# Performance work log

Measured on AMD Instinct MI355X. Metric: run time of the kernel, lower is better.

## Reference

```python
import jax, jax.numpy as jnp
import numpy as np

B, S, F_IN = 128, 64, 32          # batch, window_size (seq), input features
E, L, H, HOR = 96, 4, 8, 24       # embed_dim, num_layers, num_heads, horizon
E2 = 2 * E                        # attention hidden size (conv output channels)
D = E2 // H                       # head_dim
FLAT = S * E2                     # flattened fc feature size


def _ln(x, scale, offset, eps=1e-5):
    mu = jnp.mean(x, axis=-1, keepdims=True)
    var = jnp.var(x, axis=-1, keepdims=True)
    return (x - mu) * jax.lax.rsqrt(var + eps) * scale + offset


def _gattention(h, qk_w, qk_b, mass_w, mass_b, v_w, v_b):
    b, s, _ = h.shape
    qk = (h @ qk_w + qk_b).reshape(b, s, H, D).transpose(0, 2, 1, 3)  # (b,h,s,d)
    # d^2 = |qi|^2 + |qj|^2 - 2 qi.qj  (GEMM identity; exact value is >= 0)
    sq = jnp.sum(qk * qk, axis=-1)                                    # (b,h,s)
    dot = jnp.einsum('bhid,bhjd->bhij', qk, qk)
    d2 = jnp.maximum(sq[:, :, :, None] + sq[:, :, None, :] - 2.0 * dot, 0.0) + 1e-6
    mass = jax.nn.softplus(h @ mass_w + mass_b).transpose(0, 2, 1)    # (b,h,s)
    scores = (mass[:, :, :, None] * mass[:, :, None, :]) / d2
    w = jax.nn.softmax(scores, axis=-1)
    v = (h @ v_w + v_b).reshape(b, s, H, D).transpose(0, 2, 1, 3)
    out = jnp.einsum('bhij,bhjd->bhid', w, v)
    return out.transpose(0, 2, 1, 3).reshape(b, s, E2)


def setup_inputs() -> dict:
    key = jax.random.key(0)
    ks = iter(jax.random.split(key, 16))
    r = lambda *shape: jax.random.normal(next(ks), shape, jnp.float32) * 0.02
    return dict(
        x=jax.random.normal(next(ks), (B, S, F_IN), jnp.float32),
        proj_w=r(F_IN, E), proj_b=jnp.zeros((E,), jnp.float32),
        ln0_s=jnp.ones((E,), jnp.float32), ln0_o=jnp.zeros((E,), jnp.float32),
        conv_w=r(4, 4, E, E2), conv_b=jnp.zeros((E2,), jnp.float32),
        ln1_s=jnp.ones((E2,), jnp.float32), ln1_o=jnp.zeros((E2,), jnp.float32),
        qk_w=r(L, E2, E2), qk_b=jnp.zeros((L, E2), jnp.float32),
        mass_w=r(L, E2, H), mass_b=jnp.zeros((L, H), jnp.float32),
        v_w=r(L, E2, E2), v_b=jnp.zeros((L, E2), jnp.float32),
        norm_s=jnp.ones((L, E2), jnp.float32), norm_o=jnp.zeros((L, E2), jnp.float32),
        mlp_w1=r(E2, 4 * E), mlp_b1=jnp.zeros((4 * E,), jnp.float32),
        mlp_w2=r(4 * E, E2), mlp_b2=jnp.zeros((E2,), jnp.float32),
        fc_w=r(FLAT, FLAT), fc_b=jnp.zeros((FLAT,), jnp.float32),
        ln2_s=jnp.ones((FLAT,), jnp.float32), ln2_o=jnp.zeros((FLAT,), jnp.float32),
        out_w=r(FLAT, HOR), out_b=jnp.zeros((HOR,), jnp.float32),
    )


def reference(x, proj_w, proj_b, ln0_s, ln0_o, conv_w, conv_b, ln1_s, ln1_o,
              qk_w, qk_b, mass_w, mass_b, v_w, v_b, norm_s, norm_o,
              mlp_w1, mlp_b1, mlp_w2, mlp_b2, fc_w, fc_b, ln2_s, ln2_o,
              out_w, out_b):
    # proj: Linear -> LN -> gelu
    h = jax.nn.gelu(_ln(x @ proj_w + proj_b, ln0_s, ln0_o))            # (B,S,E)
    # hk.Conv2D on rank-3 input: treated as a single unbatched HWC image
    y = jax.lax.conv_general_dilated(
        h[None], conv_w, window_strides=(1, 1), padding='SAME',
        dimension_numbers=('NHWC', 'HWIO', 'NHWC'))[0] + conv_b        # (B,S,E2)
    h = jax.nn.gelu(_ln(y, ln1_s, ln1_o))
    for i in range(L):
        a = _gattention(h, qk_w[i], qk_b[i], mass_w[i], mass_b[i], v_w[i], v_b[i])
        h = jax.nn.gelu(_ln(h + a, norm_s[i], norm_o[i]))
    h = h + (jax.nn.gelu(h @ mlp_w1 + mlp_b1) @ mlp_w2 + mlp_b2)
    f = _ln(jax.nn.gelu(h.reshape(B, FLAT) @ fc_w + fc_b), ln2_s, ln2_o)
    return f @ out_w + out_b                                           # (B,HOR)
```

## Files before the change

kernel.cpp:

```cpp
#include <hip/hip_runtime.h>
#include <math.h>

typedef __attribute__((ext_vector_type(8))) short short8;
typedef __attribute__((ext_vector_type(4))) float f32x4;

__device__ __forceinline__ unsigned short bf16_rne(float f) {
  union { float f; unsigned u; } x; x.f = f;
  unsigned r = x.u + 0x7FFFu + ((x.u >> 16) & 1u);
  return (unsigned short)(r >> 16);
}

__device__ __forceinline__ float gelu_f(float x) {
  float z = 0.7978845608028654f * (x + 0.044715f * x * x * x);
  z = fminf(fmaxf(z, -15.f), 15.f);
  float e = __expf(2.f * z);
  float th = (e - 1.f) / (e + 1.f);
  return 0.5f * x * (1.f + th);
}

__device__ __forceinline__ float softplus_f(float x) {
  return (x > 15.f) ? x : log1pf(__expf(x));
}

__device__ __forceinline__ float wave_sum(float v) {
  #pragma unroll
  for (int off = 32; off > 0; off >>= 1) v += __shfl_down(v, off, 64);
  return v;
}

__global__ __launch_bounds__(256) void proj_kern(
    const float* __restrict__ x, const float* __restrict__ w,
    const float* __restrict__ b, const float* __restrict__ s,
    const float* __restrict__ o, unsigned short* __restrict__ h0bf)
{
  int t = threadIdx.x, wave = t >> 6, l = t & 63;
  size_t row = (size_t)blockIdx.x * 4 + wave;
  const float* xr = x + row * 32;
  bool has2 = (l < 32);
  int c1 = l, c2 = has2 ? 64 + l : 0;
  float v1 = b[c1], v2 = b[c2];
  #pragma unroll
  for (int k = 0; k < 32; ++k) {
    float xv = xr[k];
    v1 += xv * w[k * 96 + c1];
    v2 += xv * w[k * 96 + c2];
  }
  if (!has2) v2 = 0.f;
  float sum = wave_sum(v1 + v2);
  float ssq = wave_sum(v1 * v1 + v2 * v2);
  sum = __shfl(sum, 0, 64); ssq = __shfl(ssq, 0, 64);
  float mu = sum / 96.f, var = ssq / 96.f - mu * mu;
  float inv = rsqrtf(var + 1e-5f);
  float f1 = gelu_f((v1 - mu) * inv * s[c1] + o[c1]);
  h0bf[row * 96 + c1] = bf16_rne(f1);
  if (has2) {
    float f2 = gelu_f((v2 - mu) * inv * s[c2] + o[c2]);
    h0bf[row * 96 + c2] = bf16_rne(f2);
  }
}

__global__ __launch_bounds__(256) void cvtw_kern(
    const float* __restrict__ cw, unsigned short* __restrict__ cwT)
{
  int e = blockIdx.x * 256 + threadIdx.x;
  int co = e % 192, rest = e / 192;
  int ci = rest % 96, tap = rest / 96;
  cwT[((size_t)tap * 192 + co) * 96 + ci] = bf16_rne(cw[e]);
}

__global__ __launch_bounds__(256) void conv_kern(
    const unsigned short* __restrict__ h0bf, const unsigned short* __restrict__ cwT,
    const float* __restrict__ cb, float* __restrict__ y)
{
  __shared__ unsigned short As[12 * 64 * 8];
  __shared__ unsigned short Ws[12 * 64 * 8];
  int t = threadIdx.x;
  int i = blockIdx.x;
  int n0 = blockIdx.y * 64;
  int wave = t >> 6, lane = t & 63, quad = lane >> 4, l16 = lane & 15;
  f32x4 zero4 = {0.f, 0.f, 0.f, 0.f};
  f32x4 acc[4];
  #pragma unroll
  for (int nt = 0; nt < 4; ++nt) acc[nt] = zero4;
  for (int tap = 0; tap < 16; ++tap) {
    int kh = tap >> 2, kw = tap & 3;
    int si = i + kh - 1;
    if (si < 0 || si >= 128) continue;
    {
      int j = t & 63, g = t >> 6;
      int sj = j + kw - 1;
      bool ok = (sj >= 0 && sj < 64);
      #pragma unroll
      for (int q = 0; q < 3; ++q) {
        int kb = g + 4 * q;
        short8 v = {0,0,0,0,0,0,0,0};
        if (ok) v = *(const short8*)(h0bf + (size_t)(si * 64 + sj) * 96 + kb * 8);
        *(short8*)(As + (kb * 64 + j) * 8) = v;
      }
    }
    {
      int n = t & 63, g = t >> 6;
      #pragma unroll
      for (int q = 0; q < 3; ++q) {
        int kb = g + 4 * q;
        *(short8*)(Ws + (kb * 64 + n) * 8) =
            *(const short8*)(cwT + ((size_t)tap * 192 + n0 + n) * 96 + kb * 8);
      }
    }
    __syncthreads();
    #pragma unroll
    for (int ks = 0; ks < 3; ++ks) {
      int kbq = ks * 4 + quad;
      short8 a = *(const short8*)(As + (kbq * 64 + wave * 16 + l16) * 8);
      #pragma unroll
      for (int nt = 0; nt < 4; ++nt) {
        short8 b = *(const short8*)(Ws + (kbq * 64 + nt * 16 + l16) * 8);
        acc[nt] = __builtin_amdgcn_mfma_f32_16x16x32_bf16(a, b, acc[nt], 0, 0, 0);
      }
    }
    __syncthreads();
  }
  #pragma unroll
  for (int nt = 0; nt < 4; ++nt) {
    int col = n0 + nt * 16 + l16;
    float bv = cb[col];
    #pragma unroll
    for (int r = 0; r < 4; ++r) {
      int row = wave * 16 + quad * 4 + r;
      y[(size_t)(i * 64 + row) * 192 + col] = acc[nt][r] + bv;
    }
  }
}

__global__ __launch_bounds__(256) void ln_act_kern(
    const float* __restrict__ y, const float* __restrict__ res,
    const float* __restrict__ s, const float* __restrict__ o,
    float* __restrict__ h32, unsigned short* __restrict__ hbf)
{
  int t = threadIdx.x, wave = t >> 6, l = t & 63;
  size_t base = ((size_t)blockIdx.x * 4 + wave) * 192;
  float v0 = y[base + l], v1 = y[base + 64 + l], v2 = y[base + 128 + l];
  if (res) { v0 += res[base + l]; v1 += res[base + 64 + l]; v2 += res[base + 128 + l]; }
  float sum = wave_sum(v0 + v1 + v2);
  float ssq = wave_sum(v0 * v0 + v1 * v1 + v2 * v2);
  sum = __shfl(sum, 0, 64); ssq = __shfl(ssq, 0, 64);
  float mu = sum * (1.f / 192.f);
  float var = ssq * (1.f / 192.f) - mu * mu;
  float inv = rsqrtf(var + 1e-5f);
  float f0 = gelu_f((v0 - mu) * inv * s[l] + o[l]);
  float f1 = gelu_f((v1 - mu) * inv * s[64 + l] + o[64 + l]);
  float f2 = gelu_f((v2 - mu) * inv * s[128 + l] + o[128 + l]);
  h32[base + l] = f0; h32[base + 64 + l] = f1; h32[base + 128 + l] = f2;
  hbf[base + l] = bf16_rne(f0); hbf[base + 64 + l] = bf16_rne(f1); hbf[base + 128 + l] = bf16_rne(f2);
}

__global__ __launch_bounds__(256) void gemm_qkv(
    const unsigned short* __restrict__ A,
    const float* __restrict__ qw, const float* __restrict__ qb,
    const float* __restrict__ vw, const float* __restrict__ vb,
    float* __restrict__ t_qk, float* __restrict__ t_v)
{
  __shared__ unsigned short As[8 * 64 * 8];
  __shared__ unsigned short Ws[8 * 64 * 8];
  int t = threadIdx.x;
  int m0 = blockIdx.x * 64;
  int ny = blockIdx.y;
  const float* W; const float* bias; float* outF; int n0;
  if (ny < 3) { W = qw; bias = qb; outF = t_qk; n0 = ny * 64; }
  else        { W = vw; bias = vb; outF = t_v;  n0 = (ny - 3) * 64; }
  int wave = t >> 6, lane = t & 63, quad = lane >> 4, l16 = lane & 15;
  f32x4 zero4 = {0.f, 0.f, 0.f, 0.f};
  f32x4 acc[4];
  #pragma unroll
  for (int nt = 0; nt < 4; ++nt) acc[nt] = zero4;
  for (int k0 = 0; k0 < 192; k0 += 64) {
    {
      int kb = t & 7, m = t >> 3;
      #pragma unroll
      for (int r = 0; r < 2; ++r) {
        int mm = m + r * 32;
        *(short8*)(As + (kb * 64 + mm) * 8) =
            *(const short8*)(A + (size_t)(m0 + mm) * 192 + k0 + kb * 8);
      }
    }
    {
      int n = t & 63, g = t >> 6;
      #pragma unroll
      for (int q = 0; q < 2; ++q) {
        int kb = g + 4 * q;
        short8 v;
        #pragma unroll
        for (int jj = 0; jj < 8; ++jj)
          v[jj] = (short)bf16_rne(W[(size_t)(k0 + kb * 8 + jj) * 192 + n0 + n]);
        *(short8*)(Ws + (kb * 64 + n) * 8) = v;
      }
    }
    __syncthreads();
    #pragma unroll
    for (int ks = 0; ks < 2; ++ks) {
      short8 a = *(const short8*)(As + ((ks * 4 + quad) * 64 + wave * 16 + l16) * 8);
      #pragma unroll
      for (int nt = 0; nt < 4; ++nt) {
        short8 b = *(const short8*)(Ws + ((ks * 4 + quad) * 64 + nt * 16 + l16) * 8);
        acc[nt] = __builtin_amdgcn_mfma_f32_16x16x32_bf16(a, b, acc[nt], 0, 0, 0);
      }
    }
    __syncthreads();
  }
  #pragma unroll
  for (int nt = 0; nt < 4; ++nt) {
    int col = n0 + nt * 16 + l16;
    float bv = bias[col];
    #pragma unroll
    for (int r = 0; r < 4; ++r) {
      int row = m0 + wave * 16 + quad * 4 + r;
      outF[(size_t)row * 192 + col] = acc[nt][r] + bv;
    }
  }
}

__global__ __launch_bounds__(256) void gemm_small(
    const unsigned short* __restrict__ A, int lda,
    const float* __restrict__ W, int ldw,
    const float* __restrict__ bias, const float* __restrict__ res,
    float* __restrict__ outF, unsigned short* __restrict__ outB,
    int K, int ldo, int act)
{
  __shared__ unsigned short As[8 * 64 * 8];
  __shared__ unsigned short Ws[8 * 64 * 8];
  int t = threadIdx.x;
  int m0 = blockIdx.x * 64, n0 = blockIdx.y * 64;
  int wave = t >> 6, lane = t & 63, quad = lane >> 4, l16 = lane & 15;
  f32x4 zero4 = {0.f, 0.f, 0.f, 0.f};
  f32x4 acc[4];
  #pragma unroll
  for (int nt = 0; nt < 4; ++nt) acc[nt] = zero4;
  for (int k0 = 0; k0 < K; k0 += 64) {
    {
      int kb = t & 7, m = t >> 3;
      #pragma unroll
      for (int r = 0; r < 2; ++r) {
        int mm = m + r * 32;
        *(short8*)(As + (kb * 64 + mm) * 8) =
            *(const short8*)(A + (size_t)(m0 + mm) * lda + k0 + kb * 8);
      }
    }
    {
      int n = t & 63, g = t >> 6;
      #pragma unroll
      for (int q = 0; q < 2; ++q) {
        int kb = g + 4 * q;
        short8 v;
        #pragma unroll
        for (int jj = 0; jj < 8; ++jj)
          v[jj] = (short)bf16_rne(W[(size_t)(k0 + kb * 8 + jj) * ldw + n0 + n]);
        *(short8*)(Ws + (kb * 64 + n) * 8) = v;
      }
    }
    __syncthreads();
    #pragma unroll
    for (int ks = 0; ks < 2; ++ks) {
      short8 a = *(const short8*)(As + ((ks * 4 + quad) * 64 + wave * 16 + l16) * 8);
      #pragma unroll
      for (int nt = 0; nt < 4; ++nt) {
        short8 b = *(const short8*)(Ws + ((ks * 4 + quad) * 64 + nt * 16 + l16) * 8);
        acc[nt] = __builtin_amdgcn_mfma_f32_16x16x32_bf16(a, b, acc[nt], 0, 0, 0);
      }
    }
    __syncthreads();
  }
  #pragma unroll
  for (int nt = 0; nt < 4; ++nt) {
    int col = n0 + nt * 16 + l16;
    float bv = bias[col];
    #pragma unroll
    for (int r = 0; r < 4; ++r) {
      int row = m0 + wave * 16 + quad * 4 + r;
      float v = acc[nt][r] + bv;
      if (act) v = gelu_f(v);
      if (res) v += res[(size_t)row * ldo + col];
      if (outF) outF[(size_t)row * ldo + col] = v;
      if (outB) outB[(size_t)row * ldo + col] = bf16_rne(v);
    }
  }
}

__global__ __launch_bounds__(256) void attn_core(
    const float* __restrict__ qk, const float* __restrict__ v,
    const float* __restrict__ h32, const float* __restrict__ mw,
    const float* __restrict__ mb, float* __restrict__ att)
{
  __shared__ float qs[64][25], vs[64][25];
  __shared__ float sqv[64], mm[64], inv64[64];
  __shared__ float sc[64][65];
  int t = threadIdx.x;
  int b = blockIdx.x >> 3, hh = blockIdx.x & 7;
  size_t base = ((size_t)b * 64) * 192 + hh * 24;
  for (int e = t; e < 1536; e += 256) {
    int r = e / 24, d = e - r * 24;
    qs[r][d] = qk[base + (size_t)r * 192 + d];
    vs[r][d] = v[base + (size_t)r * 192 + d];
  }
  {
    int r = t >> 2, q = t & 3;
    const float* hr = h32 + ((size_t)b * 64 + r) * 192 + q * 48;
    float dot = 0.f;
    #pragma unroll
    for (int kk = 0; kk < 48; ++kk) dot += hr[kk] * mw[(q * 48 + kk) * 8 + hh];
    dot += __shfl_down(dot, 2, 4);
    dot += __shfl_down(dot, 1, 4);
    if (q == 0) mm[r] = softplus_f(dot + mb[hh]);
  }
  __syncthreads();
  if (t < 64) {
    float s = 0.f;
    #pragma unroll
    for (int d = 0; d < 24; ++d) s += qs[t][d] * qs[t][d];
    sqv[t] = s;
  }
  __syncthreads();
  {
    int i = t & 63, g = t >> 6;
    float qi[24];
    #pragma unroll
    for (int d = 0; d < 24; ++d) qi[d] = qs[i][d];
    float sqi = sqv[i], mi = mm[i];
    for (int jj = 0; jj < 16; ++jj) {
      int j = g + jj * 4;
      float dot = 0.f;
      #pragma unroll
      for (int d = 0; d < 24; ++d) dot += qi[d] * qs[j][d];
      float d2 = fmaxf(sqi + sqv[j] - 2.f * dot, 0.f) + 1e-6f;
      sc[i][j] = mi * mm[j] / d2;
    }
  }
  __syncthreads();
  if (t < 64) {
    float mx = -1e30f;
    for (int j = 0; j < 64; ++j) mx = fmaxf(mx, sc[t][j]);
    float sum = 0.f;
    for (int j = 0; j < 64; ++j) { float e = __expf(sc[t][j] - mx); sc[t][j] = e; sum += e; }
    inv64[t] = 1.f / sum;
  }
  __syncthreads();
  {
    int i = t & 63, g = t >> 6;
    float a6[6] = {0,0,0,0,0,0};
    for (int j = 0; j < 64; ++j) {
      float w = sc[i][j];
      #pragma unroll
      for (int dd = 0; dd < 6; ++dd) a6[dd] += w * vs[j][g * 6 + dd];
    }
    float inv = inv64[i];
    #pragma unroll
    for (int dd = 0; dd < 6; ++dd)
      att[base + (size_t)i * 192 + g * 6 + dd] = a6[dd] * inv;
  }
}

__global__ __launch_bounds__(256) void gemm_fc(
    const unsigned short* __restrict__ A, const float* __restrict__ W,
    float* __restrict__ part)
{
  __shared__ unsigned short As[8 * 128 * 8];
  __shared__ unsigned short Bs[8 * 64 * 8];
  int t = threadIdx.x;
  int n0 = blockIdx.x * 64;
  int split = blockIdx.y;
  int wave = t >> 6, lane = t & 63, quad = lane >> 4, l16 = lane & 15;
  int wm = wave * 32;
  int a_kb = t & 7, a_m = t >> 3;
  int w_n4 = t & 15, w_kr = t >> 4;
  f32x4 zero4 = {0.f, 0.f, 0.f, 0.f};
  f32x4 acc[2][4];
  #pragma unroll
  for (int mt = 0; mt < 2; ++mt)
    #pragma unroll
    for (int nt = 0; nt < 4; ++nt) acc[mt][nt] = zero4;
  int k0 = split * 3072;
  for (int it = 0; it < 48; ++it, k0 += 64) {
    #pragma unroll
    for (int r = 0; r < 4; ++r) {
      int mm2 = a_m + r * 32;
      *(short8*)(As + (a_kb * 128 + mm2) * 8) =
          *(const short8*)(A + (size_t)mm2 * 12288 + k0 + a_kb * 8);
    }
    #pragma unroll
    for (int r = 0; r < 4; ++r) {
      int k = w_kr + 16 * r;
      f32x4 wv = *(const f32x4*)(W + (size_t)(k0 + k) * 12288 + n0 + w_n4 * 4);
      int kb = k >> 3, kj = k & 7;
      #pragma unroll
      for (int j = 0; j < 4; ++j)
        Bs[(kb * 64 + w_n4 * 4 + j) * 8 + kj] = bf16_rne(wv[j]);
    }
    __syncthreads();
    #pragma unroll
    for (int ks = 0; ks < 2; ++ks) {
      int kq = ks * 4 + quad;
      short8 a[2], b[4];
      #pragma unroll
      for (int mt = 0; mt < 2; ++mt)
        a[mt] = *(const short8*)(As + (kq * 128 + wm + mt * 16 + l16) * 8);
      #pragma unroll
      for (int nt = 0; nt < 4; ++nt)
        b[nt] = *(const short8*)(Bs + (kq * 64 + nt * 16 + l16) * 8);
      #pragma unroll
      for (int mt = 0; mt < 2; ++mt)
        #pragma unroll
        for (int nt = 0; nt < 4; ++nt)
          acc[mt][nt] = __builtin_amdgcn_mfma_f32_16x16x32_bf16(a[mt], b[nt], acc[mt][nt], 0, 0, 0);
    }
    __syncthreads();
  }
  float* po = part + (size_t)split * 128 * 12288;
  #pragma unroll
  for (int mt = 0; mt < 2; ++mt) {
    #pragma unroll
    for (int nt = 0; nt < 4; ++nt) {
      int col = n0 + nt * 16 + l16;
      #pragma unroll
      for (int r = 0; r < 4; ++r) {
        int row = wm + mt * 16 + quad * 4 + r;
        po[(size_t)row * 12288 + col] = acc[mt][nt][r];
      }
    }
  }
}

__global__ __launch_bounds__(256) void reduce_fc(
    const float* __restrict__ part, const float* __restrict__ fb,
    float* __restrict__ g)
{
  int i4 = blockIdx.x * 256 + threadIdx.x;
  const int S4 = 128 * 12288 / 4;
  const f32x4* p = (const f32x4*)part;
  f32x4 v = p[i4] + p[i4 + S4] + p[i4 + 2 * S4] + p[i4 + 3 * S4];
  int n = (i4 * 4) % 12288;
  f32x4 bb = *(const f32x4*)(fb + n);
  f32x4 o;
  #pragma unroll
  for (int c = 0; c < 4; ++c) o[c] = gelu_f(v[c] + bb[c]);
  ((f32x4*)g)[i4] = o;
}

__global__ __launch_bounds__(256) void final_kern(
    const float* __restrict__ g, const float* __restrict__ s,
    const float* __restrict__ o, const float* __restrict__ ow,
    const float* __restrict__ ob, float* __restrict__ out)
{
  int m = blockIdx.x, t = threadIdx.x;
  const float* gr = g + (size_t)m * 12288;
  float s1 = 0.f, s2 = 0.f;
  for (int k4 = t; k4 < 3072; k4 += 256) {
    f32x4 v = ((const f32x4*)gr)[k4];
    s1 += v[0] + v[1] + v[2] + v[3];
    s2 += v[0]*v[0] + v[1]*v[1] + v[2]*v[2] + v[3]*v[3];
  }
  s1 = wave_sum(s1); s2 = wave_sum(s2);
  __shared__ float a1[4], a2[4];
  int wv = t >> 6, ln = t & 63;
  if (ln == 0) { a1[wv] = s1; a2[wv] = s2; }
  __syncthreads();
  float sum = a1[0] + a1[1] + a1[2] + a1[3];
  float ssq = a2[0] + a2[1] + a2[2] + a2[3];
  float mu = sum / 12288.f, var = ssq / 12288.f - mu * mu;
  float inv = rsqrtf(var + 1e-5f);
  f32x4 acc6[6];
  #pragma unroll
  for (int j = 0; j < 6; ++j) acc6[j] = (f32x4){0.f,0.f,0.f,0.f};
  for (int k = t; k < 12288; k += 256) {
    float f = (gr[k] - mu) * inv * s[k] + o[k];
    const f32x4* owr = (const f32x4*)(ow + (size_t)k * 24);
    #pragma unroll
    for (int j = 0; j < 6; ++j) acc6[j] += f * owr[j];
  }
  __shared__ float red[4][24];
  #pragma unroll
  for (int j = 0; j < 6; ++j)
    #pragma unroll
    for (int c = 0; c < 4; ++c) {
      float v = wave_sum(acc6[j][c]);
      if (ln == 0) red[wv][j * 4 + c] = v;
    }
  __syncthreads();
  if (t < 24) out[m * 24 + t] = red[0][t] + red[1][t] + red[2][t] + red[3][t] + ob[t];
}

extern "C" void kernel_launch(void* const* d_in, const int* in_sizes, int n_in,
                              void* d_out, int out_size, void* d_ws, size_t ws_size,
                              hipStream_t stream) {
  const float* x      = (const float*)d_in[0];
  const float* proj_w = (const float*)d_in[1];
  const float* proj_b = (const float*)d_in[2];
  const float* ln0_s  = (const float*)d_in[3];
  const float* ln0_o  = (const float*)d_in[4];
  const float* conv_w = (const float*)d_in[5];
  const float* conv_b = (const float*)d_in[6];
  const float* ln1_s  = (const float*)d_in[7];
  const float* ln1_o  = (const float*)d_in[8];
  const float* qk_w   = (const float*)d_in[9];
  const float* qk_b   = (const float*)d_in[10];
  const float* mass_w = (const float*)d_in[11];
  const float* mass_b = (const float*)d_in[12];
  const float* v_w    = (const float*)d_in[13];
  const float* v_b    = (const float*)d_in[14];
  const float* norm_s = (const float*)d_in[15];
  const float* norm_o = (const float*)d_in[16];
  const float* mlp_w1 = (const float*)d_in[17];
  const float* mlp_b1 = (const float*)d_in[18];
  const float* mlp_w2 = (const float*)d_in[19];
  const float* mlp_b2 = (const float*)d_in[20];
  const float* fc_w   = (const float*)d_in[21];
  const float* fc_b   = (const float*)d_in[22];
  const float* ln2_s  = (const float*)d_in[23];
  const float* ln2_o  = (const float*)d_in[24];
  const float* out_w  = (const float*)d_in[25];
  const float* out_b  = (const float*)d_in[26];
  float* out = (float*)d_out;

  char* ws = (char*)d_ws;
  unsigned short* h0bf = (unsigned short*)(ws + 0);
  float* h32           = (float*)(ws + 1572864);
  unsigned short* hbf  = (unsigned short*)(ws + 7864320);
  unsigned short* cwT  = (unsigned short*)(ws + 11010048);
  char* sc = ws + 11599872;
  float* t_qk  = (float*)(sc);
  float* t_v   = (float*)(sc + 6291456);
  float* t_att = (float*)(sc + 12582912);
  unsigned short* hid_bf = (unsigned short*)(sc + 18874368);
  float* partials = (float*)sc;
  float* gbuf = h32;

  proj_kern<<<2048, 256, 0, stream>>>(x, proj_w, proj_b, ln0_s, ln0_o, h0bf);
  cvtw_kern<<<1152, 256, 0, stream>>>(conv_w, cwT);
  conv_kern<<<dim3(128, 3), 256, 0, stream>>>(h0bf, cwT, conv_b, t_att);
  ln_act_kern<<<2048, 256, 0, stream>>>(t_att, nullptr, ln1_s, ln1_o, h32, hbf);
  for (int l = 0; l < 4; ++l) {
    gemm_qkv<<<dim3(128, 6), 256, 0, stream>>>(hbf, qk_w + l * 36864, qk_b + l * 192,
        v_w + l * 36864, v_b + l * 192, t_qk, t_v);
    attn_core<<<1024, 256, 0, stream>>>(t_qk, t_v, h32, mass_w + l * 1536,
                                        mass_b + l * 8, t_att);
    ln_act_kern<<<2048, 256, 0, stream>>>(t_att, h32, norm_s + l * 192,
                                          norm_o + l * 192, h32, hbf);
  }
  gemm_small<<<dim3(128, 6), 256, 0, stream>>>(hbf, 192, mlp_w1, 384, mlp_b1,
      nullptr, (float*)nullptr, hid_bf, 192, 384, 1);
  gemm_small<<<dim3(128, 3), 256, 0, stream>>>(hid_bf, 384, mlp_w2, 192, mlp_b2,
      h32, h32, hbf, 384, 192, 0);
  gemm_fc<<<dim3(192, 4), 256, 0, stream>>>(hbf, fc_w, partials);
  reduce_fc<<<1536, 256, 0, stream>>>(partials, fc_b, gbuf);
  final_kern<<<128, 256, 0, stream>>>(gbuf, ln2_s, ln2_o, out_w, out_b, out);
}
```

Baseline: 1.150 ms.

## Fuse QKV projection and attention per layer, merge pre and final kernels

New measurement: 1.101 ms. 1.04x faster.

```diff
diff --git a/kernel.cpp b/kernel.cpp
--- a/kernel.cpp
+++ b/kernel.cpp
@@ -28,11 +28,19 @@
   return v;
 }
 
-__global__ __launch_bounds__(256) void proj_kern(
+__global__ __launch_bounds__(256) void pre_kern(
     const float* __restrict__ x, const float* __restrict__ w,
     const float* __restrict__ b, const float* __restrict__ s,
-    const float* __restrict__ o, unsigned short* __restrict__ h0bf)
-{
+    const float* __restrict__ o, unsigned short* __restrict__ h0bf,
+    const float* __restrict__ cw, unsigned short* __restrict__ cwT)
+{
+  if (blockIdx.x >= 2048) {
+    int e = (blockIdx.x - 2048) * 256 + threadIdx.x;
+    int co = e % 192, rest = e / 192;
+    int ci = rest % 96, tap = rest / 96;
+    cwT[((size_t)tap * 192 + co) * 96 + ci] = bf16_rne(cw[e]);
+    return;
+  }
   int t = threadIdx.x, wave = t >> 6, l = t & 63;
   size_t row = (size_t)blockIdx.x * 4 + wave;
   const float* xr = x + row * 32;
@@ -57,15 +65,6 @@
     float f2 = gelu_f((v2 - mu) * inv * s[c2] + o[c2]);
     h0bf[row * 96 + c2] = bf16_rne(f2);
   }
-}
-
-__global__ __launch_bounds__(256) void cvtw_kern(
-    const float* __restrict__ cw, unsigned short* __restrict__ cwT)
-{
-  int e = blockIdx.x * 256 + threadIdx.x;
-  int co = e % 192, rest = e / 192;
-  int ci = rest % 96, tap = rest / 96;
-  cwT[((size_t)tap * 192 + co) * 96 + ci] = bf16_rne(cw[e]);
 }
 
 __global__ __launch_bounds__(256) void conv_kern(
@@ -154,69 +153,225 @@
   hbf[base + l] = bf16_rne(f0); hbf[base + 64 + l] = bf16_rne(f1); hbf[base + 128 + l] = bf16_rne(f2);
 }
 
-__global__ __launch_bounds__(256) void gemm_qkv(
-    const unsigned short* __restrict__ A,
+__device__ __forceinline__ void stage_w(
+    unsigned short* Wt, const float* qw, const float* vw, const float* mw,
+    int half, int k0, int t)
+{
+  for (int c = t; c < 1664; c += 256) {
+    int kb = c / 208, n = c - kb * 208;
+    short8 v8;
+    if (n < 192) {
+      const float* src = (n < 96) ? (qw + half * 96 + n) : (vw + half * 96 + n - 96);
+      #pragma unroll
+      for (int jj = 0; jj < 8; ++jj)
+        v8[jj] = (short)bf16_rne(src[(size_t)(k0 + kb * 8 + jj) * 192]);
+    } else if (n < 196) {
+      const float* src = mw + half * 4 + (n - 192);
+      #pragma unroll
+      for (int jj = 0; jj < 8; ++jj)
+        v8[jj] = (short)bf16_rne(src[(size_t)(k0 + kb * 8 + jj) * 8]);
+    } else {
+      v8 = (short8){0,0,0,0,0,0,0,0};
+    }
+    *(short8*)(Wt + c * 8) = v8;
+  }
+}
+
+__global__ __launch_bounds__(256) void layer_attn(
+    const unsigned short* __restrict__ hbf,
     const float* __restrict__ qw, const float* __restrict__ qb,
     const float* __restrict__ vw, const float* __restrict__ vb,
-    float* __restrict__ t_qk, float* __restrict__ t_v)
-{
-  __shared__ unsigned short As[8 * 64 * 8];
-  __shared__ unsigned short Ws[8 * 64 * 8];
+    const float* __restrict__ mw, const float* __restrict__ mb,
+    float* __restrict__ att)
+{
+  extern __shared__ char smem[];
+  unsigned short* qk_lds = (unsigned short*)smem;
+  unsigned short* v_ldsp = (unsigned short*)(smem + 16384);
+  unsigned short* w_bfp  = (unsigned short*)(smem + 32768);
+  float* mmp = (float*)(smem + 65536);
+  float* sqp = (float*)(smem + 66560);
+  unsigned short* A_bf = (unsigned short*)smem;
+  unsigned short* Wt   = (unsigned short*)(smem + 24576);
+
   int t = threadIdx.x;
-  int m0 = blockIdx.x * 64;
-  int ny = blockIdx.y;
-  const float* W; const float* bias; float* outF; int n0;
-  if (ny < 3) { W = qw; bias = qb; outF = t_qk; n0 = ny * 64; }
-  else        { W = vw; bias = vb; outF = t_v;  n0 = (ny - 3) * 64; }
-  int wave = t >> 6, lane = t & 63, quad = lane >> 4, l16 = lane & 15;
-  f32x4 zero4 = {0.f, 0.f, 0.f, 0.f};
-  f32x4 acc[4];
-  #pragma unroll
-  for (int nt = 0; nt < 4; ++nt) acc[nt] = zero4;
-  for (int k0 = 0; k0 < 192; k0 += 64) {
-    {
-      int kb = t & 7, m = t >> 3;
-      #pragma unroll
-      for (int r = 0; r < 2; ++r) {
-        int mm = m + r * 32;
-        *(short8*)(As + (kb * 64 + mm) * 8) =
-            *(const short8*)(A + (size_t)(m0 + mm) * 192 + k0 + kb * 8);
-      }
-    }
-    {
-      int n = t & 63, g = t >> 6;
-      #pragma unroll
-      for (int q = 0; q < 2; ++q) {
-        int kb = g + 4 * q;
-        short8 v;
+  int bb = blockIdx.x >> 1, half = blockIdx.x & 1;
+  int wv = t >> 6, lane = t & 63, quad = lane >> 4, l16 = lane & 15;
+
+  for (int c = t; c < 1536; c += 256) {
+    int kb = c >> 6, m = c & 63;
+    *(short8*)(A_bf + c * 8) =
+        *(const short8*)(hbf + ((size_t)bb * 64 + m) * 192 + kb * 8);
+  }
+  stage_w(Wt, qw, vw, mw, half, 0, t);
+  __syncthreads();
+  f32x4 acc[13];
+  #pragma unroll
+  for (int i = 0; i < 13; ++i) acc[i] = (f32x4){0.f,0.f,0.f,0.f};
+  for (int kt = 0; kt < 3; ++kt) {
+    #pragma unroll
+    for (int ks = 0; ks < 2; ++ks) {
+      int kq = ks * 4 + quad;
+      short8 a = *(const short8*)(A_bf + ((kt * 8 + kq) * 64 + wv * 16 + l16) * 8);
+      #pragma unroll
+      for (int nt = 0; nt < 13; ++nt) {
+        short8 b = *(const short8*)(Wt + (kq * 208 + nt * 16 + l16) * 8);
+        acc[nt] = __builtin_amdgcn_mfma_f32_16x16x32_bf16(a, b, acc[nt], 0, 0, 0);
+      }
+    }
+    if (kt < 2) {
+      __syncthreads();
+      stage_w(Wt, qw, vw, mw, half, (kt + 1) * 64, t);
+      __syncthreads();
+    }
+  }
+  __syncthreads();
+
+  {
+    int zh = t >> 6, zs = t & 63;
+    *(short8*)(qk_lds + ((zh * 4 + 3) * 64 + zs) * 8) = (short8){0,0,0,0,0,0,0,0};
+  }
+  int row = wv * 16 + quad * 4;
+  #pragma unroll
+  for (int nt = 0; nt < 6; ++nt) {
+    int n = nt * 16 + l16;
+    int hl = n / 24, d = n - hl * 24;
+    float bqv = qb[half * 96 + n];
+    #pragma unroll
+    for (int r = 0; r < 4; ++r)
+      qk_lds[((hl * 4 + (d >> 3)) * 64 + row + r) * 8 + (d & 7)] =
+          bf16_rne(acc[nt][r] + bqv);
+  }
+  #pragma unroll
+  for (int nt = 0; nt < 6; ++nt) {
+    int n = nt * 16 + l16;
+    int hl = n / 24, d = n - hl * 24;
+    float bvv = vb[half * 96 + n];
+    #pragma unroll
+    for (int r = 0; r < 4; ++r) {
+      int sidx = row + r;
+      v_ldsp[((hl * 8 + (sidx >> 3)) * 32 + d) * 8 + (sidx & 7)] =
+          bf16_rne(acc[nt + 6][r] + bvv);
+    }
+  }
+  if (l16 < 4) {
+    float mbv = mb[half * 4 + l16];
+    #pragma unroll
+    for (int r = 0; r < 4; ++r)
+      mmp[(row + r) * 4 + l16] = softplus_f(acc[12][r] + mbv);
+  }
+  __syncthreads();
+
+  const unsigned short* qh = qk_lds + (wv * 4) * 64 * 8;
+  short8 frag[4];
+  #pragma unroll
+  for (int x2 = 0; x2 < 4; ++x2)
+    frag[x2] = *(const short8*)(qh + (quad * 64 + x2 * 16 + l16) * 8);
+  f32x4 s16[4][4];
+  #pragma unroll
+  for (int mt = 0; mt < 4; ++mt)
+    #pragma unroll
+    for (int nt = 0; nt < 4; ++nt)
+      s16[mt][nt] = __builtin_amdgcn_mfma_f32_16x16x32_bf16(
+          frag[mt], frag[nt], (f32x4){0.f,0.f,0.f,0.f}, 0, 0, 0);
+  float* sqh = sqp + wv * 64;
+  #pragma unroll
+  for (int mt = 0; mt < 4; ++mt)
+    #pragma unroll
+    for (int r = 0; r < 4; ++r)
+      if (l16 == quad * 4 + r) sqh[mt * 16 + l16] = s16[mt][mt][r];
+  __syncthreads();
+  f32x4 sqr[4], mr[4];
+  float sqc[4], mc[4];
+  #pragma unroll
+  for (int mt = 0; mt < 4; ++mt) {
+    sqr[mt] = *(const f32x4*)(sqh + mt * 16 + quad * 4);
+    #pragma unroll
+    for (int r = 0; r < 4; ++r) mr[mt][r] = mmp[(mt * 16 + quad * 4 + r) * 4 + wv];
+  }
+  #pragma unroll
+  for (int nt = 0; nt < 4; ++nt) {
+    sqc[nt] = sqh[nt * 16 + l16];
+    mc[nt]  = mmp[(nt * 16 + l16) * 4 + wv];
+  }
+  #pragma unroll
+  for (int mt = 0; mt < 4; ++mt)
+    #pragma unroll
+    for (int nt = 0; nt < 4; ++nt)
+      #pragma unroll
+      for (int r = 0; r < 4; ++r) {
+        float d2 = fmaxf(sqr[mt][r] + sqc[nt] - 2.f * s16[mt][nt][r], 0.f) + 1e-6f;
+        s16[mt][nt][r] = mr[mt][r] * mc[nt] / d2;
+      }
+  f32x4 inv4[4];
+  #pragma unroll
+  for (int mt = 0; mt < 4; ++mt)
+    #pragma unroll
+    for (int r = 0; r < 4; ++r) {
+      float mx = fmaxf(fmaxf(s16[mt][0][r], s16[mt][1][r]),
+                       fmaxf(s16[mt][2][r], s16[mt][3][r]));
+      #pragma unroll
+      for (int off = 1; off < 16; off <<= 1) mx = fmaxf(mx, __shfl_xor(mx, off, 64));
+      float sm = 0.f;
+      #pragma unroll
+      for (int nt = 0; nt < 4; ++nt) {
+        float e = __expf(s16[mt][nt][r] - mx);
+        s16[mt][nt][r] = e;
+        sm += e;
+      }
+      #pragma unroll
+      for (int off = 1; off < 16; off <<= 1) sm += __shfl_xor(sm, off, 64);
+      inv4[mt][r] = 1.f / sm;
+    }
+
+  unsigned short* wb = w_bfp + wv * (8 * 64 * 8);
+  #pragma unroll
+  for (int mt = 0; mt < 4; ++mt)
+    #pragma unroll
+    for (int nt = 0; nt < 4; ++nt)
+      #pragma unroll
+      for (int r = 0; r < 4; ++r) {
+        int si = mt * 16 + quad * 4 + r, sj = nt * 16 + l16;
+        wb[((sj >> 3) * 64 + si) * 8 + (sj & 7)] = bf16_rne(s16[mt][nt][r]);
+      }
+  __syncthreads();
+
+  const unsigned short* vh = v_ldsp + wv * (8 * 32 * 8);
+  f32x4 o2[4][2];
+  #pragma unroll
+  for (int mt = 0; mt < 4; ++mt)
+    #pragma unroll
+    for (int nt = 0; nt < 2; ++nt) o2[mt][nt] = (f32x4){0.f,0.f,0.f,0.f};
+  #pragma unroll
+  for (int ks = 0; ks < 2; ++ks) {
+    int kq = ks * 4 + quad;
+    short8 aw[4], bv2[2];
+    #pragma unroll
+    for (int mt = 0; mt < 4; ++mt)
+      aw[mt] = *(const short8*)(wb + (kq * 64 + mt * 16 + l16) * 8);
+    #pragma unroll
+    for (int nt = 0; nt < 2; ++nt)
+      bv2[nt] = *(const short8*)(vh + (kq * 32 + nt * 16 + l16) * 8);
+    #pragma unroll
+    for (int mt = 0; mt < 4; ++mt)
+      #pragma unroll
+      for (int nt = 0; nt < 2; ++nt)
+        o2[mt][nt] = __builtin_amdgcn_mfma_f32_16x16x32_bf16(aw[mt], bv2[nt], o2[mt][nt], 0, 0, 0);
+  }
+  int hg = half * 4 + wv;
+  size_t obase = ((size_t)bb * 64) * 192 + hg * 24;
+  #pragma unroll
+  for (int mt = 0; mt < 4; ++mt)
+    #pragma unroll
+    for (int nt = 0; nt < 2; ++nt) {
+      int col = nt * 16 + l16;
+      if (col < 24) {
         #pragma unroll
-        for (int jj = 0; jj < 8; ++jj)
-          v[jj] = (short)bf16_rne(W[(size_t)(k0 + kb * 8 + jj) * 192 + n0 + n]);
-        *(short8*)(Ws + (kb * 64 + n) * 8) = v;
-      }
-    }
-    __syncthreads();
-    #pragma unroll
-    for (int ks = 0; ks < 2; ++ks) {
-      short8 a = *(const short8*)(As + ((ks * 4 + quad) * 64 + wave * 16 + l16) * 8);
-      #pragma unroll
-      for (int nt = 0; nt < 4; ++nt) {
-        short8 b = *(const short8*)(Ws + ((ks * 4 + quad) * 64 + nt * 16 + l16) * 8);
-        acc[nt] = __builtin_amdgcn_mfma_f32_16x16x32_bf16(a, b, acc[nt], 0, 0, 0);
-      }
-    }
-    __syncthreads();
-  }
-  #pragma unroll
-  for (int nt = 0; nt < 4; ++nt) {
-    int col = n0 + nt * 16 + l16;
-    float bv = bias[col];
-    #pragma unroll
-    for (int r = 0; r < 4; ++r) {
-      int row = m0 + wave * 16 + quad * 4 + r;
-      outF[(size_t)row * 192 + col] = acc[nt][r] + bv;
-    }
-  }
+        for (int r = 0; r < 4; ++r) {
+          int sidx = mt * 16 + quad * 4 + r;
+          att[obase + (size_t)sidx * 192 + col] = o2[mt][nt][r] * inv4[mt][r];
+        }
+      }
+    }
 }
 
 __global__ __launch_bounds__(256) void gemm_small(
@@ -282,79 +437,6 @@
       if (outF) outF[(size_t)row * ldo + col] = v;
       if (outB) outB[(size_t)row * ldo + col] = bf16_rne(v);
     }
-  }
-}
-
-__global__ __launch_bounds__(256) void attn_core(
-    const float* __restrict__ qk, const float* __restrict__ v,
-    const float* __restrict__ h32, const float* __restrict__ mw,
-    const float* __restrict__ mb, float* __restrict__ att)
-{
-  __shared__ float qs[64][25], vs[64][25];
-  __shared__ float sqv[64], mm[64], inv64[64];
-  __shared__ float sc[64][65];
-  int t = threadIdx.x;
-  int b = blockIdx.x >> 3, hh = blockIdx.x & 7;
-  size_t base = ((size_t)b * 64) * 192 + hh * 24;
-  for (int e = t; e < 1536; e += 256) {
-    int r = e / 24, d = e - r * 24;
-    qs[r][d] = qk[base + (size_t)r * 192 + d];
-    vs[r][d] = v[base + (size_t)r * 192 + d];
-  }
-  {
-    int r = t >> 2, q = t & 3;
-    const float* hr = h32 + ((size_t)b * 64 + r) * 192 + q * 48;
-    float dot = 0.f;
-    #pragma unroll
-    for (int kk = 0; kk < 48; ++kk) dot += hr[kk] * mw[(q * 48 + kk) * 8 + hh];
-    dot += __shfl_down(dot, 2, 4);
-    dot += __shfl_down(dot, 1, 4);
-    if (q == 0) mm[r] = softplus_f(dot + mb[hh]);
-  }
-  __syncthreads();
-  if (t < 64) {
-    float s = 0.f;
-    #pragma unroll
-    for (int d = 0; d < 24; ++d) s += qs[t][d] * qs[t][d];
-    sqv[t] = s;
-  }
-  __syncthreads();
-  {
-    int i = t & 63, g = t >> 6;
-    float qi[24];
-    #pragma unroll
-    for (int d = 0; d < 24; ++d) qi[d] = qs[i][d];
-    float sqi = sqv[i], mi = mm[i];
-    for (int jj = 0; jj < 16; ++jj) {
-      int j = g + jj * 4;
-      float dot = 0.f;
-      #pragma unroll
-      for (int d = 0; d < 24; ++d) dot += qi[d] * qs[j][d];
-      float d2 = fmaxf(sqi + sqv[j] - 2.f * dot, 0.f) + 1e-6f;
-      sc[i][j] = mi * mm[j] / d2;
-    }
-  }
-  __syncthreads();
-  if (t < 64) {
-    float mx = -1e30f;
-    for (int j = 0; j < 64; ++j) mx = fmaxf(mx, sc[t][j]);
-    float sum = 0.f;
-    for (int j = 0; j < 64; ++j) { float e = __expf(sc[t][j] - mx); sc[t][j] = e; sum += e; }
-    inv64[t] = 1.f / sum;
-  }
-  __syncthreads();
-  {
-    int i = t & 63, g = t >> 6;
-    float a6[6] = {0,0,0,0,0,0};
-    for (int j = 0; j < 64; ++j) {
-      float w = sc[i][j];
-      #pragma unroll
-      for (int dd = 0; dd < 6; ++dd) a6[dd] += w * vs[j][g * 6 + dd];
-    }
-    float inv = inv64[i];
-    #pragma unroll
-    for (int dd = 0; dd < 6; ++dd)
-      att[base + (size_t)i * 192 + g * 6 + dd] = a6[dd] * inv;
   }
 }
 
@@ -377,24 +459,35 @@
   for (int mt = 0; mt < 2; ++mt)
     #pragma unroll
     for (int nt = 0; nt < 4; ++nt) acc[mt][nt] = zero4;
-  int k0 = split * 3072;
-  for (int it = 0; it < 48; ++it, k0 += 64) {
+  int kk = split * 3072;
+  short8 aR[4]; f32x4 wR[4];
+  #pragma unroll
+  for (int r = 0; r < 4; ++r)
+    aR[r] = *(const short8*)(A + (size_t)(a_m + r * 32) * 12288 + kk + a_kb * 8);
+  #pragma unroll
+  for (int r = 0; r < 4; ++r)
+    wR[r] = *(const f32x4*)(W + (size_t)(kk + w_kr + 16 * r) * 12288 + n0 + w_n4 * 4);
+  for (int it = 0; it < 48; ++it) {
+    #pragma unroll
+    for (int r = 0; r < 4; ++r)
+      *(short8*)(As + (a_kb * 128 + a_m + r * 32) * 8) = aR[r];
     #pragma unroll
     for (int r = 0; r < 4; ++r) {
-      int mm2 = a_m + r * 32;
-      *(short8*)(As + (a_kb * 128 + mm2) * 8) =
-          *(const short8*)(A + (size_t)mm2 * 12288 + k0 + a_kb * 8);
-    }
-    #pragma unroll
-    for (int r = 0; r < 4; ++r) {
-      int k = w_kr + 16 * r;
-      f32x4 wv = *(const f32x4*)(W + (size_t)(k0 + k) * 12288 + n0 + w_n4 * 4);
-      int kb = k >> 3, kj = k & 7;
+      int k = w_kr + 16 * r, kb = k >> 3, kj = k & 7;
       #pragma unroll
       for (int j = 0; j < 4; ++j)
-        Bs[(kb * 64 + w_n4 * 4 + j) * 8 + kj] = bf16_rne(wv[j]);
+        Bs[(kb * 64 + w_n4 * 4 + j) * 8 + kj] = bf16_rne(wR[r][j]);
     }
     __syncthreads();
+    if (it < 47) {
+      int kn = kk + 64;
+      #pragma unroll
+      for (int r = 0; r < 4; ++r)
+        aR[r] = *(const short8*)(A + (size_t)(a_m + r * 32) * 12288 + kn + a_kb * 8);
+      #pragma unroll
+      for (int r = 0; r < 4; ++r)
+        wR[r] = *(const f32x4*)(W + (size_t)(kn + w_kr + 16 * r) * 12288 + n0 + w_n4 * 4);
+    }
     #pragma unroll
     for (int ks = 0; ks < 2; ++ks) {
       int kq = ks * 4 + quad;
@@ -412,6 +505,7 @@
           acc[mt][nt] = __builtin_amdgcn_mfma_f32_16x16x32_bf16(a[mt], b[nt], acc[mt][nt], 0, 0, 0);
     }
     __syncthreads();
+    kk += 64;
   }
   float* po = part + (size_t)split * 128 * 12288;
   #pragma unroll
@@ -428,37 +522,30 @@
   }
 }
 
-__global__ __launch_bounds__(256) void reduce_fc(
+__global__ __launch_bounds__(256) void final_kern(
     const float* __restrict__ part, const float* __restrict__ fb,
-    float* __restrict__ g)
-{
-  int i4 = blockIdx.x * 256 + threadIdx.x;
-  const int S4 = 128 * 12288 / 4;
-  const f32x4* p = (const f32x4*)part;
-  f32x4 v = p[i4] + p[i4 + S4] + p[i4 + 2 * S4] + p[i4 + 3 * S4];
-  int n = (i4 * 4) % 12288;
-  f32x4 bb = *(const f32x4*)(fb + n);
-  f32x4 o;
-  #pragma unroll
-  for (int c = 0; c < 4; ++c) o[c] = gelu_f(v[c] + bb[c]);
-  ((f32x4*)g)[i4] = o;
-}
-
-__global__ __launch_bounds__(256) void final_kern(
-    const float* __restrict__ g, const float* __restrict__ s,
-    const float* __restrict__ o, const float* __restrict__ ow,
-    const float* __restrict__ ob, float* __restrict__ out)
-{
+    const float* __restrict__ s, const float* __restrict__ o,
+    const float* __restrict__ ow, const float* __restrict__ ob,
+    float* __restrict__ out)
+{
+  __shared__ float gls[12288];
+  __shared__ float a1[4], a2[4];
+  __shared__ float red[4][24];
   int m = blockIdx.x, t = threadIdx.x;
-  const float* gr = g + (size_t)m * 12288;
+  const f32x4* p0 = (const f32x4*)(part + (size_t)m * 12288);
+  const size_t S4 = (size_t)128 * 12288 / 4;
   float s1 = 0.f, s2 = 0.f;
   for (int k4 = t; k4 < 3072; k4 += 256) {
-    f32x4 v = ((const f32x4*)gr)[k4];
-    s1 += v[0] + v[1] + v[2] + v[3];
-    s2 += v[0]*v[0] + v[1]*v[1] + v[2]*v[2] + v[3]*v[3];
+    f32x4 v = p0[k4] + p0[k4 + S4] + p0[k4 + 2 * S4] + p0[k4 + 3 * S4];
+    f32x4 bb = *(const f32x4*)(fb + k4 * 4);
+    f32x4 g;
+    #pragma unroll
+    for (int c = 0; c < 4; ++c) g[c] = gelu_f(v[c] + bb[c]);
+    *(f32x4*)(gls + k4 * 4) = g;
+    s1 += g[0] + g[1] + g[2] + g[3];
+    s2 += g[0]*g[0] + g[1]*g[1] + g[2]*g[2] + g[3]*g[3];
   }
   s1 = wave_sum(s1); s2 = wave_sum(s2);
-  __shared__ float a1[4], a2[4];
   int wv = t >> 6, ln = t & 63;
   if (ln == 0) { a1[wv] = s1; a2[wv] = s2; }
   __syncthreads();
@@ -470,12 +557,11 @@
   #pragma unroll
   for (int j = 0; j < 6; ++j) acc6[j] = (f32x4){0.f,0.f,0.f,0.f};
   for (int k = t; k < 12288; k += 256) {
-    float f = (gr[k] - mu) * inv * s[k] + o[k];
+    float f = (gls[k] - mu) * inv * s[k] + o[k];
     const f32x4* owr = (const f32x4*)(ow + (size_t)k * 24);
     #pragma unroll
     for (int j = 0; j < 6; ++j) acc6[j] += f * owr[j];
   }
-  __shared__ float red[4][24];
   #pragma unroll
   for (int j = 0; j < 6; ++j)
     #pragma unroll
@@ -525,22 +611,19 @@
   unsigned short* hbf  = (unsigned short*)(ws + 7864320);
   unsigned short* cwT  = (unsigned short*)(ws + 11010048);
   char* sc = ws + 11599872;
-  float* t_qk  = (float*)(sc);
-  float* t_v   = (float*)(sc + 6291456);
   float* t_att = (float*)(sc + 12582912);
   unsigned short* hid_bf = (unsigned short*)(sc + 18874368);
   float* partials = (float*)sc;
-  float* gbuf = h32;
-
-  proj_kern<<<2048, 256, 0, stream>>>(x, proj_w, proj_b, ln0_s, ln0_o, h0bf);
-  cvtw_kern<<<1152, 256, 0, stream>>>(conv_w, cwT);
+
+  pre_kern<<<3200, 256, 0, stream>>>(x, proj_w, proj_b, ln0_s, ln0_o, h0bf,
+                                     conv_w, cwT);
   conv_kern<<<dim3(128, 3), 256, 0, stream>>>(h0bf, cwT, conv_b, t_att);
   ln_act_kern<<<2048, 256, 0, stream>>>(t_att, nullptr, ln1_s, ln1_o, h32, hbf);
   for (int l = 0; l < 4; ++l) {
-    gemm_qkv<<<dim3(128, 6), 256, 0, stream>>>(hbf, qk_w + l * 36864, qk_b + l * 192,
-        v_w + l * 36864, v_b + l * 192, t_qk, t_v);
-    attn_core<<<1024, 256, 0, stream>>>(t_qk, t_v, h32, mass_w + l * 1536,
-                                        mass_b + l * 8, t_att);
+    layer_attn<<<256, 256, 67584, stream>>>(hbf,
+        qk_w + l * 36864, qk_b + l * 192,
+        v_w + l * 36864, v_b + l * 192,
+        mass_w + l * 1536, mass_b + l * 8, t_att);
     ln_act_kern<<<2048, 256, 0, stream>>>(t_att, h32, norm_s + l * 192,
                                           norm_o + l * 192, h32, hbf);
   }
@@ -549,6 +632,5 @@
   gemm_small<<<dim3(128, 3), 256, 0, stream>>>(hid_bf, 384, mlp_w2, 192, mlp_b2,
       h32, h32, hbf, 384, 192, 0);
   gemm_fc<<<dim3(192, 4), 256, 0, stream>>>(hbf, fc_w, partials);
-  reduce_fc<<<1536, 256, 0, stream>>>(partials, fc_b, gbuf);
-  final_kern<<<128, 256, 0, stream>>>(gbuf, ln2_s, ln2_o, out_w, out_b, out);
-}
+  final_kern<<<128, 256, 0, stream>>>(partials, fc_b, ln2_s, ln2_o, out_w, out_b, out);
+}
```
